# Kernel tuning notes

Measured on AMD Instinct MI355X. Metric: run time of the kernel, lower is better.

Reference implementation:

```python
import jax, jax.numpy as jnp
import numpy as np

N_HEAD = 16
N_EMBD = 1024
HEAD_DIM = N_EMBD // N_HEAD
ROPE_BASE = 10000.0


def _rms_norm(x):
    # F.rms_norm with eps=None uses dtype eps
    eps = jnp.finfo(x.dtype).eps
    ms = jnp.mean(jnp.square(x), axis=-1, keepdims=True)
    return x * jax.lax.rsqrt(ms + eps)


def _rope_tables(T, dtype):
    inv_freq = 1.0 / (ROPE_BASE ** (jnp.arange(0, HEAD_DIM, 2, dtype=jnp.float32) / HEAD_DIM))
    t = jnp.arange(T, dtype=jnp.float32)
    freqs = jnp.outer(t, inv_freq)  # [T, D/2]
    cos = jnp.cos(freqs).astype(dtype)[None, :, None, :]  # [1,T,1,D/2]
    sin = jnp.sin(freqs).astype(dtype)[None, :, None, :]
    return cos, sin


def _apply_rotary(x, cos, sin):
    d = x.shape[-1] // 2
    x1, x2 = x[..., :d], x[..., d:]
    y1 = x1 * cos + x2 * sin
    y2 = -x1 * sin + x2 * cos
    return jnp.concatenate([y1, y2], axis=-1).astype(x.dtype)


def setup_inputs() -> dict:
    key = jax.random.key(0)
    ks = jax.random.split(key, 7)
    B, T, C = 4, 2048, N_EMBD
    s = 0.02
    return {
        "x": jax.random.normal(ks[0], (B, T, C), dtype=jnp.float32),
        "v1": jax.random.normal(ks[1], (B, T, C), dtype=jnp.float32),
        "Wq": jax.random.normal(ks[2], (C, C), dtype=jnp.float32) * s,
        "Wk": jax.random.normal(ks[3], (C, C), dtype=jnp.float32) * s,
        "Wv": jax.random.normal(ks[4], (C, C), dtype=jnp.float32) * s,
        "Wproj": jax.random.normal(ks[5], (C, C), dtype=jnp.float32) * s,
        "lamb": jnp.float32(0.5),
    }


def reference(x, v1, Wq, Wk, Wv, Wproj, lamb):
    B, T, C = x.shape
    H, D = N_HEAD, HEAD_DIM
    q = (x @ Wq.T).reshape(B, T, H, D)
    k = (x @ Wk.T).reshape(B, T, H, D)
    v = (x @ Wv.T).reshape(B, T, H, D)
    # value-lambda residual mix
    v = (1.0 - lamb) * v + lamb * v1.reshape(B, T, H, D)
    # RMSNorm then RoPE on q, k
    cos, sin = _rope_tables(T, x.dtype)
    q = _apply_rotary(_rms_norm(q), cos, sin)
    k = _apply_rotary(_rms_norm(k), cos, sin)
    # causal SDPA
    scale = 1.0 / jnp.sqrt(jnp.float32(D)).astype(x.dtype)
    scores = jnp.einsum("bthd,bshd->bhts", q, k) * scale  # [B,H,T,T]
    causal = jnp.tril(jnp.ones((T, T), dtype=bool))
    scores = jnp.where(causal[None, None], scores, jnp.finfo(scores.dtype).min)
    attn = jax.nn.softmax(scores, axis=-1)
    y = jnp.einsum("bhts,bshd->bthd", attn, v).reshape(B, T, C)
    y = y @ Wproj.T
    return (y, v1)
```

## Files before the change

kernel.cpp:

```cpp
#include <hip/hip_runtime.h>
#include <hip/hip_bf16.h>

typedef __bf16 bf16x8 __attribute__((ext_vector_type(8)));
typedef __bf16 bf16x4 __attribute__((ext_vector_type(4)));
typedef float  f32x4  __attribute__((ext_vector_type(4)));

#define B_ 4
#define T_ 2048
#define H_ 16
#define D_ 64
#define C_ 1024
#define M_ 8192
#define NE_ ((size_t)M_ * C_)

__global__ void probe_dtype(const unsigned short* __restrict__ x,
                            int* __restrict__ flag)
{
  __shared__ float red[256];
  float m = 0.0f;
  for (int i = threadIdx.x; i < 4096; i += 256) {
    unsigned int u = ((unsigned int)x[i]) << 16;
    float v = fabsf(__uint_as_float(u));
    if (!(v <= 1e30f)) v = 1e31f;
    m = fmaxf(m, v);
  }
  red[threadIdx.x] = m;
  __syncthreads();
  for (int s = 128; s > 0; s >>= 1) {
    if (threadIdx.x < s) red[threadIdx.x] = fmaxf(red[threadIdx.x], red[threadIdx.x + s]);
    __syncthreads();
  }
  if (threadIdx.x == 0) *flag = (red[0] > 100.0f) ? 1 : 0;
}

__device__ __forceinline__ float load1_adapt(const void* p, size_t idx, int f)
{
  if (f) return ((const float*)p)[idx];
  return __bfloat162float(((const __hip_bfloat16*)p)[idx]);
}

__global__ __launch_bounds__(256) void cvt_bf16(
    const int* __restrict__ flagp, const void* __restrict__ src,
    __bf16* __restrict__ dst, int n)
{
  const int f = *flagp;
  for (size_t i = ((size_t)blockIdx.x * 256 + threadIdx.x) * 8; i < (size_t)n;
       i += (size_t)gridDim.x * 2048) {
    bf16x8 r;
    if (f) {
      const float* pf = (const float*)src + i;
      float4 a = *(const float4*)pf;
      float4 b = *(const float4*)(pf + 4);
      r[0] = (__bf16)a.x; r[1] = (__bf16)a.y; r[2] = (__bf16)a.z; r[3] = (__bf16)a.w;
      r[4] = (__bf16)b.x; r[5] = (__bf16)b.y; r[6] = (__bf16)b.z; r[7] = (__bf16)b.w;
    } else {
      r = *(const bf16x8*)((const __bf16*)src + i);
    }
    *(bf16x8*)(dst + i) = r;
  }
}

__device__ __forceinline__ void g2lds16(const __bf16* g, __bf16* l)
{
  __builtin_amdgcn_global_load_lds(
      (const __attribute__((address_space(1))) void*)g,
      (__attribute__((address_space(3))) void*)l, 16, 0, 0);
}

__global__ __launch_bounds__(256) void gemm128(
    const __bf16* __restrict__ A, const __bf16* __restrict__ Bm,
    void* __restrict__ C, int M, int N, int K,
    const int* __restrict__ flagp, int adaptive)
{
  __shared__ __bf16 As[128][64];
  __shared__ __bf16 Bs[128][64];

  const int tid  = threadIdx.x;
  const int wv   = tid >> 6;
  const int lane = tid & 63;
  const int n16  = lane & 15;
  const int quad = lane >> 4;
  const int wm = (wv & 1) * 64, wn = (wv >> 1) * 64;

  const int nwgx = gridDim.x;
  const int id   = blockIdx.y * nwgx + blockIdx.x;
  const int cpx  = (nwgx * gridDim.y) >> 3;
  const int swz  = (id & 7) * cpx + (id >> 3);
  const int m0 = (swz % nwgx) * 128, n0 = (swz / nwgx) * 128;

  f32x4 acc[4][4];
#pragma unroll
  for (int i = 0; i < 4; i++)
#pragma unroll
    for (int j = 0; j < 4; j++) acc[i][j] = (f32x4){0.f, 0.f, 0.f, 0.f};

  const int trow = tid >> 3;
  const int tcol = (tid & 7) * 8;

  for (int k0 = 0; k0 < K; k0 += 64) {
#pragma unroll
    for (int p = 0; p < 4; p++) {
      g2lds16(A  + (size_t)(m0 + trow + p * 32) * K + k0 + tcol,
              &As[trow + p * 32][tcol]);
      g2lds16(Bm + (size_t)(n0 + trow + p * 32) * K + k0 + tcol,
              &Bs[trow + p * 32][tcol]);
    }
    __syncthreads();

#pragma unroll
    for (int kk = 0; kk < 2; kk++) {
      bf16x8 af[4], bf[4];
#pragma unroll
      for (int i = 0; i < 4; i++) {
        af[i] = *(const bf16x8*)&As[wm + i * 16 + n16][kk * 32 + quad * 8];
        bf[i] = *(const bf16x8*)&Bs[wn + i * 16 + n16][kk * 32 + quad * 8];
      }
#pragma unroll
      for (int i = 0; i < 4; i++)
#pragma unroll
        for (int j = 0; j < 4; j++)
          acc[i][j] = __builtin_amdgcn_mfma_f32_16x16x32_bf16(af[i], bf[j],
                                                              acc[i][j], 0, 0, 0);
    }
    __syncthreads();
  }

  const int f = adaptive ? *flagp : 0;
  const int rb = quad * 4;
#pragma unroll
  for (int i = 0; i < 4; i++)
#pragma unroll
    for (int j = 0; j < 4; j++)
#pragma unroll
      for (int r = 0; r < 4; r++) {
        const size_t idx = (size_t)(m0 + wm + i * 16 + rb + r) * N
                           + n0 + wn + j * 16 + n16;
        if (f) ((float*)C)[idx] = acc[i][j][r];
        else   ((__bf16*)C)[idx] = (__bf16)acc[i][j][r];
      }
}

__global__ __launch_bounds__(256) void fuse_rope_vmix(
    const int* __restrict__ flagp,
    __hip_bfloat16* __restrict__ q,
    __hip_bfloat16* __restrict__ k,
    __hip_bfloat16* __restrict__ v,
    const void* __restrict__ v1,
    const void* __restrict__ lambp)
{
  const int f    = *flagp;
  const int task = blockIdx.x * 4 + (threadIdx.x >> 6);
  const int lane = threadIdx.x & 63;
  const int h  = task & 15;
  const int bt = task >> 4;
  const int t  = bt & (T_ - 1);
  const size_t base = (size_t)bt * C_ + h * D_ + lane;

  const int j = lane & 31;
  const float inv = expf(-(float)j * (9.2103403719761836f / 32.0f));
  const float ang = (float)t * inv;
  const float cs = cosf(ang), sn = sinf(ang);
  const float EPS = 0.0078125f;

  {
    float xv = __bfloat162float(q[base]);
    float ss = xv * xv;
#pragma unroll
    for (int off = 32; off >= 1; off >>= 1) ss += __shfl_xor(ss, off);
    float r  = rsqrtf(ss * (1.0f / 64.0f) + EPS);
    float xn = xv * r;
    float pr = __shfl_xor(xn, 32);
    float yv = (lane < 32) ? (xn * cs + pr * sn) : (pr * -sn + xn * cs);
    q[base] = __float2bfloat16(yv);
  }
  {
    float xv = __bfloat162float(k[base]);
    float ss = xv * xv;
#pragma unroll
    for (int off = 32; off >= 1; off >>= 1) ss += __shfl_xor(ss, off);
    float r  = rsqrtf(ss * (1.0f / 64.0f) + EPS);
    float xn = xv * r;
    float pr = __shfl_xor(xn, 32);
    float yv = (lane < 32) ? (xn * cs + pr * sn) : (pr * -sn + xn * cs);
    k[base] = __float2bfloat16(yv);
  }
  {
    float lam = load1_adapt(lambp, 0, f);
    float vv  = __bfloat162float(v[base]);
    float v1v = load1_adapt(v1, base, f);
    v[base] = __float2bfloat16((1.0f - lam) * vv + lam * v1v);
  }
}

__global__ __launch_bounds__(256) void attn_mfma(
    const __bf16* q,
    const __bf16* __restrict__ k,
    const __bf16* __restrict__ v,
    __bf16* y)
{
  __shared__ alignas(16) __bf16 Ks[64][72];
  __shared__ alignas(16) __bf16 VTs[64][88];
  __shared__ alignas(16) __bf16 Ps[4][16][76];

  const int tid  = threadIdx.x;
  const int wv   = tid >> 6;
  const int lane = tid & 63;
  const int n16  = lane & 15;
  const int quad = lane >> 4;
  const int b = blockIdx.y >> 4, h = blockIdx.y & 15;
  const int q0 = (gridDim.x - 1 - blockIdx.x) * 128;
  const size_t hb = (size_t)b * T_ * C_ + h * D_;

  const __bf16 one_ = (__bf16)1.0f;
  const bf16x8 onev = {one_, one_, one_, one_, one_, one_, one_, one_};

  bf16x8 aq[2][2];
#pragma unroll
  for (int rt = 0; rt < 2; rt++) {
    const size_t qoff = hb + (size_t)(q0 + wv * 32 + rt * 16 + n16) * C_;
    aq[rt][0] = *(const bf16x8*)(q + qoff + quad * 8);
    aq[rt][1] = *(const bf16x8*)(q + qoff + 32 + quad * 8);
#pragma unroll
    for (int jj = 0; jj < 8; jj++) {
      aq[rt][0][jj] = (__bf16)((float)aq[rt][0][jj] * 0.125f);
      aq[rt][1][jj] = (__bf16)((float)aq[rt][1][jj] * 0.125f);
    }
  }

  f32x4 Ot[2][4];
  float l_run[2][4];
#pragma unroll
  for (int rt = 0; rt < 2; rt++)
#pragma unroll
    for (int r = 0; r < 4; r++) {
      Ot[rt][r] = (f32x4){0.f, 0.f, 0.f, 0.f};
      l_run[rt][r] = 0.0f;
    }

  const int trow = tid >> 2;
  const int tcol = (tid & 3) * 16;

  const int niter = q0 / 64 + 2;

  bf16x8 kr0, kr1, vr0, vr1;
  {
    const __bf16* ks = k + hb + (size_t)trow * C_ + tcol;
    kr0 = *(const bf16x8*)(ks);
    kr1 = *(const bf16x8*)(ks + 8);
    const __bf16* vs = v + hb + (size_t)lane * C_;
    vr0 = *(const bf16x8*)(vs + wv * 8);
    vr1 = *(const bf16x8*)(vs + (wv + 4) * 8);
    *(bf16x8*)&Ks[trow][tcol]     = kr0;
    *(bf16x8*)&Ks[trow][tcol + 8] = kr1;
#pragma unroll
    for (int jj = 0; jj < 8; jj++) VTs[wv * 8 + jj][lane] = vr0[jj];
#pragma unroll
    for (int jj = 0; jj < 8; jj++) VTs[(wv + 4) * 8 + jj][lane] = vr1[jj];
  }
  __syncthreads();

  for (int it = 0; it < niter; it++) {
    const int s0 = it * 64;
    const bool havenext = (it + 1 < niter);

    if (havenext) {
      const int sn = s0 + 64;
      const __bf16* ks = k + hb + (size_t)(sn + trow) * C_ + tcol;
      kr0 = *(const bf16x8*)(ks);
      kr1 = *(const bf16x8*)(ks + 8);
      const __bf16* vs = v + hb + (size_t)(sn + lane) * C_;
      vr0 = *(const bf16x8*)(vs + wv * 8);
      vr1 = *(const bf16x8*)(vs + (wv + 4) * 8);
    }

    if (s0 <= q0 + wv * 32 + 31) {
#pragma unroll
      for (int rt = 0; rt < 2; rt++) {
        const int rbase = q0 + wv * 32 + rt * 16;
        if (s0 <= rbase + 15) {
          f32x4 S[4];
#pragma unroll
          for (int t = 0; t < 4; t++) {
            S[t] = (f32x4){0.f, 0.f, 0.f, 0.f};
            bf16x8 b0 = *(const bf16x8*)&Ks[t * 16 + n16][quad * 8];
            bf16x8 b1 = *(const bf16x8*)&Ks[t * 16 + n16][32 + quad * 8];
            S[t] = __builtin_amdgcn_mfma_f32_16x16x32_bf16(aq[rt][0], b0, S[t], 0, 0, 0);
            S[t] = __builtin_amdgcn_mfma_f32_16x16x32_bf16(aq[rt][1], b1, S[t], 0, 0, 0);
          }

          if (s0 + 63 > rbase) {
#pragma unroll
            for (int t = 0; t < 4; t++) {
              const int sg = s0 + t * 16 + n16;
#pragma unroll
              for (int r = 0; r < 4; r++) {
                const int tg = rbase + quad * 4 + r;
                if (sg > tg) S[t][r] = -1e30f;
              }
            }
          }

#pragma unroll
          for (int r = 0; r < 4; r++) {
            float p0 = __expf(S[0][r] - 8.0f), p1 = __expf(S[1][r] - 8.0f);
            float p2 = __expf(S[2][r] - 8.0f), p3 = __expf(S[3][r] - 8.0f);
            const int prow = quad * 4 + r;
            Ps[wv][prow][n16]      = (__bf16)p0;
            Ps[wv][prow][16 + n16] = (__bf16)p1;
            Ps[wv][prow][32 + n16] = (__bf16)p2;
            Ps[wv][prow][48 + n16] = (__bf16)p3;
          }

          bf16x4 l0 = *(const bf16x4*)&Ps[wv][n16][quad * 8];
          bf16x4 l1 = *(const bf16x4*)&Ps[wv][n16][quad * 8 + 4];
          bf16x4 l2 = *(const bf16x4*)&Ps[wv][n16][32 + quad * 8];
          bf16x4 l3 = *(const bf16x4*)&Ps[wv][n16][32 + quad * 8 + 4];
          bf16x8 ap0 = __builtin_shufflevector(l0, l1, 0, 1, 2, 3, 4, 5, 6, 7);
          bf16x8 ap1 = __builtin_shufflevector(l2, l3, 0, 1, 2, 3, 4, 5, 6, 7);
#pragma unroll
          for (int t = 0; t < 4; t++) {
            bf16x8 b0 = *(const bf16x8*)&VTs[t * 16 + n16][quad * 8];
            bf16x8 b1 = *(const bf16x8*)&VTs[t * 16 + n16][32 + quad * 8];
            Ot[rt][t] = __builtin_amdgcn_mfma_f32_16x16x32_bf16(ap0, b0, Ot[rt][t], 0, 0, 0);
            Ot[rt][t] = __builtin_amdgcn_mfma_f32_16x16x32_bf16(ap1, b1, Ot[rt][t], 0, 0, 0);
          }
          f32x4 l4 = (f32x4){0.f, 0.f, 0.f, 0.f};
          l4 = __builtin_amdgcn_mfma_f32_16x16x32_bf16(ap0, onev, l4, 0, 0, 0);
          l4 = __builtin_amdgcn_mfma_f32_16x16x32_bf16(ap1, onev, l4, 0, 0, 0);
#pragma unroll
          for (int r = 0; r < 4; r++) l_run[rt][r] += l4[r];
        }
      }
    }

    __syncthreads();
    if (havenext) {
      *(bf16x8*)&Ks[trow][tcol]     = kr0;
      *(bf16x8*)&Ks[trow][tcol + 8] = kr1;
#pragma unroll
      for (int jj = 0; jj < 8; jj++) VTs[wv * 8 + jj][lane] = vr0[jj];
#pragma unroll
      for (int jj = 0; jj < 8; jj++) VTs[(wv + 4) * 8 + jj][lane] = vr1[jj];
    }
    __syncthreads();
  }

#pragma unroll
  for (int rt = 0; rt < 2; rt++) {
    float linv[4];
#pragma unroll
    for (int r = 0; r < 4; r++) linv[r] = 1.0f / l_run[rt][r];
    const int orow = q0 + wv * 32 + rt * 16 + quad * 4;
#pragma unroll
    for (int t = 0; t < 4; t++)
#pragma unroll
      for (int r = 0; r < 4; r++)
        y[hb + (size_t)(orow + r) * C_ + t * 16 + n16] =
            (__bf16)(Ot[rt][t][r] * linv[r]);
  }
}

__global__ __launch_bounds__(256) void copy_v1(
    const int* __restrict__ flagp, const void* __restrict__ v1, void* __restrict__ out)
{
  const int f = *flagp;
  const size_t nbytes = NE_ * (f ? 4u : 2u);
  const uint4* s = (const uint4*)v1;
  uint4* d = (uint4*)((char*)out + nbytes);
  const size_t n16 = nbytes / 16;
  for (size_t i = (size_t)blockIdx.x * 256 + threadIdx.x; i < n16;
       i += (size_t)gridDim.x * 256)
    d[i] = s[i];
}

extern "C" void kernel_launch(void* const* d_in, const int* in_sizes, int n_in,
                              void* d_out, int out_size, void* d_ws, size_t ws_size,
                              hipStream_t stream)
{
  const void* x    = d_in[0];
  const void* v1   = d_in[1];
  const void* Wq   = d_in[2];
  const void* Wk   = d_in[3];
  const void* Wv   = d_in[4];
  const void* Wp   = d_in[5];
  const void* lamb = d_in[6];

  __bf16* xb  = (__bf16*)d_ws;
  __bf16* qw  = xb + NE_;
  __bf16* wqb = qw + NE_;
  __bf16* wkb = wqb + (size_t)C_ * C_;
  __bf16* wvb = wkb + (size_t)C_ * C_;
  __bf16* wpb = wvb + (size_t)C_ * C_;
  int* flagp  = (int*)(wpb + (size_t)C_ * C_);
  __bf16* kw = (__bf16*)d_out;
  __bf16* vw = (__bf16*)((char*)d_out + NE_ * 2);

  probe_dtype<<<1, 256, 0, stream>>>((const unsigned short*)x, flagp);

  cvt_bf16<<<4096, 256, 0, stream>>>(flagp, x,  xb,  (int)NE_);
  cvt_bf16<<<512,  256, 0, stream>>>(flagp, Wq, wqb, C_ * C_);
  cvt_bf16<<<512,  256, 0, stream>>>(flagp, Wk, wkb, C_ * C_);
  cvt_bf16<<<512,  256, 0, stream>>>(flagp, Wv, wvb, C_ * C_);
  cvt_bf16<<<512,  256, 0, stream>>>(flagp, Wp, wpb, C_ * C_);

  dim3 gg(M_ / 128, C_ / 128);
  gemm128<<<gg, 256, 0, stream>>>(xb, wqb, qw, M_, C_, C_, flagp, 0);
  gemm128<<<gg, 256, 0, stream>>>(xb, wkb, kw, M_, C_, C_, flagp, 0);
  gemm128<<<gg, 256, 0, stream>>>(xb, wvb, vw, M_, C_, C_, flagp, 0);

  fuse_rope_vmix<<<(M_ * H_) / 4, 256, 0, stream>>>(
      flagp, (__hip_bfloat16*)qw, (__hip_bfloat16*)kw, (__hip_bfloat16*)vw,
      v1, lamb);

  attn_mfma<<<dim3(T_ / 128, B_ * H_), 256, 0, stream>>>(qw, kw, vw, qw);

  gemm128<<<gg, 256, 0, stream>>>(qw, wpb, d_out, M_, C_, C_, flagp, 1);
  copy_v1<<<8192, 256, 0, stream>>>(flagp, v1, d_out);
}
```

Measured before the change: 451.4 us.

## Transpose attention MFMA layout to keep P in registers via shuffles

```diff
diff --git a/kernel.cpp b/kernel.cpp
--- a/kernel.cpp
+++ b/kernel.cpp
@@ -4,6 +4,7 @@
 typedef __bf16 bf16x8 __attribute__((ext_vector_type(8)));
 typedef __bf16 bf16x4 __attribute__((ext_vector_type(4)));
 typedef float  f32x4  __attribute__((ext_vector_type(4)));
+typedef unsigned u32x4 __attribute__((ext_vector_type(4)));
 
 #define B_ 4
 #define T_ 2048
@@ -67,6 +68,13 @@
       (__attribute__((address_space(3))) void*)l, 16, 0, 0);
 }
 
+__device__ __forceinline__ unsigned cvtpk_bf16(float lo, float hi)
+{
+  unsigned r;
+  asm("v_cvt_pk_bf16_f32 %0, %1, %2" : "=v"(r) : "v"(lo), "v"(hi));
+  return r;
+}
+
 __global__ __launch_bounds__(256) void gemm128(
     const __bf16* __restrict__ A, const __bf16* __restrict__ Bm,
     void* __restrict__ C, int M, int N, int K,
@@ -200,7 +208,6 @@
 {
   __shared__ alignas(16) __bf16 Ks[64][72];
   __shared__ alignas(16) __bf16 VTs[64][88];
-  __shared__ alignas(16) __bf16 Ps[4][16][76];
 
   const int tid  = threadIdx.x;
   const int wv   = tid >> 6;
@@ -211,9 +218,6 @@
   const int q0 = (gridDim.x - 1 - blockIdx.x) * 128;
   const size_t hb = (size_t)b * T_ * C_ + h * D_;
 
-  const __bf16 one_ = (__bf16)1.0f;
-  const bf16x8 onev = {one_, one_, one_, one_, one_, one_, one_, one_};
-
   bf16x8 aq[2][2];
 #pragma unroll
   for (int rt = 0; rt < 2; rt++) {
@@ -228,17 +232,20 @@
   }
 
   f32x4 Ot[2][4];
-  float l_run[2][4];
-#pragma unroll
-  for (int rt = 0; rt < 2; rt++)
-#pragma unroll
-    for (int r = 0; r < 4; r++) {
-      Ot[rt][r] = (f32x4){0.f, 0.f, 0.f, 0.f};
-      l_run[rt][r] = 0.0f;
-    }
+  float l_lane[2];
+#pragma unroll
+  for (int rt = 0; rt < 2; rt++) {
+    l_lane[rt] = 0.0f;
+#pragma unroll
+    for (int t = 0; t < 4; t++) Ot[rt][t] = (f32x4){0.f, 0.f, 0.f, 0.f};
+  }
 
   const int trow = tid >> 2;
   const int tcol = (tid & 3) * 16;
+
+  const int srcA = n16 + 32 * (quad & 1);
+  const int srcB = srcA + 16;
+  const bool lowq = quad < 2;
 
   const int niter = q0 / 64 + 2;
 
@@ -279,56 +286,76 @@
         const int rbase = q0 + wv * 32 + rt * 16;
         if (s0 <= rbase + 15) {
           f32x4 S[4];
+          __builtin_amdgcn_s_setprio(1);
 #pragma unroll
           for (int t = 0; t < 4; t++) {
             S[t] = (f32x4){0.f, 0.f, 0.f, 0.f};
             bf16x8 b0 = *(const bf16x8*)&Ks[t * 16 + n16][quad * 8];
             bf16x8 b1 = *(const bf16x8*)&Ks[t * 16 + n16][32 + quad * 8];
-            S[t] = __builtin_amdgcn_mfma_f32_16x16x32_bf16(aq[rt][0], b0, S[t], 0, 0, 0);
-            S[t] = __builtin_amdgcn_mfma_f32_16x16x32_bf16(aq[rt][1], b1, S[t], 0, 0, 0);
+            S[t] = __builtin_amdgcn_mfma_f32_16x16x32_bf16(b0, aq[rt][0], S[t], 0, 0, 0);
+            S[t] = __builtin_amdgcn_mfma_f32_16x16x32_bf16(b1, aq[rt][1], S[t], 0, 0, 0);
           }
+          __builtin_amdgcn_s_setprio(0);
 
           if (s0 + 63 > rbase) {
+            const int tg = rbase + n16;
 #pragma unroll
             for (int t = 0; t < 4; t++) {
-              const int sg = s0 + t * 16 + n16;
 #pragma unroll
               for (int r = 0; r < 4; r++) {
-                const int tg = rbase + quad * 4 + r;
+                const int sg = s0 + t * 16 + quad * 4 + r;
                 if (sg > tg) S[t][r] = -1e30f;
               }
             }
           }
 
-#pragma unroll
-          for (int r = 0; r < 4; r++) {
-            float p0 = __expf(S[0][r] - 8.0f), p1 = __expf(S[1][r] - 8.0f);
-            float p2 = __expf(S[2][r] - 8.0f), p3 = __expf(S[3][r] - 8.0f);
-            const int prow = quad * 4 + r;
-            Ps[wv][prow][n16]      = (__bf16)p0;
-            Ps[wv][prow][16 + n16] = (__bf16)p1;
-            Ps[wv][prow][32 + n16] = (__bf16)p2;
-            Ps[wv][prow][48 + n16] = (__bf16)p3;
+          float p[4][4];
+#pragma unroll
+          for (int t = 0; t < 4; t++)
+#pragma unroll
+            for (int r = 0; r < 4; r++)
+              p[t][r] = __expf(S[t][r] - 8.0f);
+          l_lane[rt] += ((p[0][0] + p[0][1]) + (p[0][2] + p[0][3]))
+                      + ((p[1][0] + p[1][1]) + (p[1][2] + p[1][3]))
+                      + ((p[2][0] + p[2][1]) + (p[2][2] + p[2][3]))
+                      + ((p[3][0] + p[3][1]) + (p[3][2] + p[3][3]));
+
+          unsigned pk0[4], pk1[4];
+#pragma unroll
+          for (int t = 0; t < 4; t++) {
+            pk0[t] = cvtpk_bf16(p[t][0], p[t][1]);
+            pk1[t] = cvtpk_bf16(p[t][2], p[t][3]);
           }
 
-          bf16x4 l0 = *(const bf16x4*)&Ps[wv][n16][quad * 8];
-          bf16x4 l1 = *(const bf16x4*)&Ps[wv][n16][quad * 8 + 4];
-          bf16x4 l2 = *(const bf16x4*)&Ps[wv][n16][32 + quad * 8];
-          bf16x4 l3 = *(const bf16x4*)&Ps[wv][n16][32 + quad * 8 + 4];
-          bf16x8 ap0 = __builtin_shufflevector(l0, l1, 0, 1, 2, 3, 4, 5, 6, 7);
-          bf16x8 ap1 = __builtin_shufflevector(l2, l3, 0, 1, 2, 3, 4, 5, 6, 7);
+          bf16x8 pf[2];
+#pragma unroll
+          for (int c = 0; c < 2; c++) {
+            const int tE = 2 * c, tO = 2 * c + 1;
+            unsigned a0 = (unsigned)__shfl((int)pk0[tE], srcA);
+            unsigned a1 = (unsigned)__shfl((int)pk0[tO], srcA);
+            unsigned b0 = (unsigned)__shfl((int)pk1[tE], srcA);
+            unsigned b1 = (unsigned)__shfl((int)pk1[tO], srcA);
+            unsigned c0 = (unsigned)__shfl((int)pk0[tE], srcB);
+            unsigned c1 = (unsigned)__shfl((int)pk0[tO], srcB);
+            unsigned d0 = (unsigned)__shfl((int)pk1[tE], srcB);
+            unsigned d1 = (unsigned)__shfl((int)pk1[tO], srcB);
+            union { u32x4 u; bf16x8 b; } uw;
+            uw.u[0] = lowq ? a0 : a1;
+            uw.u[1] = lowq ? b0 : b1;
+            uw.u[2] = lowq ? c0 : c1;
+            uw.u[3] = lowq ? d0 : d1;
+            pf[c] = uw.b;
+          }
+
+          __builtin_amdgcn_s_setprio(1);
 #pragma unroll
           for (int t = 0; t < 4; t++) {
-            bf16x8 b0 = *(const bf16x8*)&VTs[t * 16 + n16][quad * 8];
-            bf16x8 b1 = *(const bf16x8*)&VTs[t * 16 + n16][32 + quad * 8];
-            Ot[rt][t] = __builtin_amdgcn_mfma_f32_16x16x32_bf16(ap0, b0, Ot[rt][t], 0, 0, 0);
-            Ot[rt][t] = __builtin_amdgcn_mfma_f32_16x16x32_bf16(ap1, b1, Ot[rt][t], 0, 0, 0);
+            bf16x8 va0 = *(const bf16x8*)&VTs[t * 16 + n16][quad * 8];
+            bf16x8 va1 = *(const bf16x8*)&VTs[t * 16 + n16][32 + quad * 8];
+            Ot[rt][t] = __builtin_amdgcn_mfma_f32_16x16x32_bf16(va0, pf[0], Ot[rt][t], 0, 0, 0);
+            Ot[rt][t] = __builtin_amdgcn_mfma_f32_16x16x32_bf16(va1, pf[1], Ot[rt][t], 0, 0, 0);
           }
-          f32x4 l4 = (f32x4){0.f, 0.f, 0.f, 0.f};
-          l4 = __builtin_amdgcn_mfma_f32_16x16x32_bf16(ap0, onev, l4, 0, 0, 0);
-          l4 = __builtin_amdgcn_mfma_f32_16x16x32_bf16(ap1, onev, l4, 0, 0, 0);
-#pragma unroll
-          for (int r = 0; r < 4; r++) l_run[rt][r] += l4[r];
+          __builtin_amdgcn_s_setprio(0);
         }
       }
     }
@@ -347,16 +374,18 @@
 
 #pragma unroll
   for (int rt = 0; rt < 2; rt++) {
-    float linv[4];
-#pragma unroll
-    for (int r = 0; r < 4; r++) linv[r] = 1.0f / l_run[rt][r];
-    const int orow = q0 + wv * 32 + rt * 16 + quad * 4;
-#pragma unroll
-    for (int t = 0; t < 4; t++)
-#pragma unroll
-      for (int r = 0; r < 4; r++)
-        y[hb + (size_t)(orow + r) * C_ + t * 16 + n16] =
-            (__bf16)(Ot[rt][t][r] * linv[r]);
+    float lt = l_lane[rt];
+    lt += __shfl_xor(lt, 16);
+    lt += __shfl_xor(lt, 32);
+    const float linv = 1.0f / lt;
+    const int qrow = q0 + wv * 32 + rt * 16 + n16;
+#pragma unroll
+    for (int t = 0; t < 4; t++) {
+      bf16x4 o;
+#pragma unroll
+      for (int r = 0; r < 4; r++) o[r] = (__bf16)(Ot[rt][t][r] * linv);
+      *(bf16x4*)(y + hb + (size_t)qrow * C_ + t * 16 + quad * 4) = o;
+    }
   }
 }
 
```

Measured after the change: 454.6 us. Within noise of the previous version (+0.7%).
